# Kernel tuning notes

Hardware: AMD Instinct MI355X
Metric: run time of the kernel (lower is better)

Reference implementation:

```python
import jax, jax.numpy as jnp
import numpy as np

N, K, T, M, P = 16, 256, 1000, 384, 2
BN_EPS = 1e-3  # keras BatchNormalization default


def setup_inputs() -> dict:
    key = jax.random.key(0)
    ks = jax.random.split(key, 16)
    inp = {
        "V": jax.random.normal(ks[0], (N, K, M), dtype=jnp.float32),
        "duration_outputs": jax.random.normal(ks[1], (N, K), dtype=jnp.float32) * 0.5,
        # ConvBatchNorm params (Conv1D(8, kernel=3, same) + BN, inference mode)
        "conv_w": jax.random.normal(ks[2], (3, M, 8), dtype=jnp.float32) * 0.05,
        "conv_b": jnp.zeros((8,), dtype=jnp.float32),
        "bn_gamma": jnp.ones((8,), dtype=jnp.float32),
        "bn_beta": jnp.zeros((8,), dtype=jnp.float32),
        "bn_mean": jnp.zeros((8,), dtype=jnp.float32),
        "bn_var": jnp.ones((8,), dtype=jnp.float32),
        # score MLP: 10 -> 16 -> 16 -> 1
        "w1": jax.random.normal(ks[3], (10, 16), dtype=jnp.float32) * 0.3,
        "b1": jnp.zeros((16,), dtype=jnp.float32),
        "w2": jax.random.normal(ks[4], (16, 16), dtype=jnp.float32) * 0.25,
        "b2": jnp.zeros((16,), dtype=jnp.float32),
        "w3": jax.random.normal(ks[5], (16, 1), dtype=jnp.float32) * 0.25,
        "b3": jnp.zeros((1,), dtype=jnp.float32),
        # auxiliary MLP: 10 -> P -> P
        "aw1": jax.random.normal(ks[6], (10, P), dtype=jnp.float32) * 0.3,
        "ab1": jnp.zeros((P,), dtype=jnp.float32),
        "aw2": jax.random.normal(ks[7], (P, P), dtype=jnp.float32) * 0.5,
        "ab2": jnp.zeros((P,), dtype=jnp.float32),
        # projection P -> M (no bias)
        "proj_w": jax.random.normal(ks[8], (P, M), dtype=jnp.float32) * 0.05,
        "max_mel_length": T,
    }
    return inp


def _forward(V, duration_outputs, conv_w, conv_b, bn_gamma, bn_beta, bn_mean,
             bn_var, w1, b1, w2, b2, w3, b3, aw1, ab1, aw2, ab2, proj_w,
             max_mel_length):
    silu = jax.nn.silu
    # durations and start/end boundaries
    durations = jax.nn.relu(jnp.exp(duration_outputs) - 1.0)      # [N,K]
    S = jnp.cumsum(durations, axis=1) - durations                 # exclusive cumsum [N,K]
    E = S + durations                                             # [N,K]
    tgrid = jnp.arange(1, max_mel_length + 1, dtype=V.dtype)      # [T]
    S_mat = tgrid[None, :, None] - S[:, None, :]                  # [N,T,K]
    E_mat = E[:, None, :] - tgrid[None, :, None]                  # [N,T,K]
    # ConvBatchNorm on V (inference: BN uses moving stats, dropout is no-op)
    conv = jax.lax.conv_general_dilated(
        V, conv_w, window_strides=(1,), padding='SAME',
        dimension_numbers=('NWC', 'WIO', 'NWC')) + conv_b         # [N,K,8]
    conv = (conv - bn_mean) * jax.lax.rsqrt(bn_var + BN_EPS) * bn_gamma + bn_beta
    conv_V = silu(conv)                                           # [N,K,8]
    n, t, k = S_mat.shape
    conv_b4 = jnp.broadcast_to(conv_V[:, None, :, :], (n, t, k, conv_V.shape[-1]))
    W_input = jnp.concatenate(
        [S_mat[..., None], E_mat[..., None], conv_b4], axis=-1)   # [N,T,K,10]
    # score MLP + softmax over K
    h = silu(W_input @ w1 + b1)
    h = silu(h @ w2 + b2)
    score = (h @ w3 + b3)[..., 0]                                 # [N,T,K]
    W = jax.nn.softmax(score, axis=-1)
    # auxiliary MLP and weighted reduction
    C = silu(silu(W_input @ aw1 + ab1) @ aw2 + ab2)               # [N,T,K,P]
    proj_C = jnp.einsum('ntk,ntkp->ntp', W, C) @ proj_w           # [N,T,M]
    O = jnp.einsum('ntk,nkm->ntm', W, V) + proj_C                 # [N,T,M]
    return O


def reference(V, duration_outputs, conv_w, conv_b, bn_gamma, bn_beta, bn_mean,
              bn_var, w1, b1, w2, b2, w3, b3, aw1, ab1, aw2, ab2, proj_w,
              max_mel_length):
    return _forward(V, duration_outputs, conv_w, conv_b, bn_gamma, bn_beta,
                    bn_mean, bn_var, w1, b1, w2, b2, w3, b3, aw1, ab1, aw2,
                    ab2, proj_w, max_mel_length)
```

## Files before the change

kernel.cpp:

```cpp
#include <hip/hip_runtime.h>

#define NN 16
#define KK 256
#define TT 1000
#define MM 384
#define TCH 8
#define TOB 28
#define TP 1008
#define TPAD 1024

typedef short bf16x8 __attribute__((ext_vector_type(8)));
typedef float f32x4 __attribute__((ext_vector_type(4)));

__device__ __forceinline__ float fast_rcp(float x) { return __builtin_amdgcn_rcpf(x); }
__device__ __forceinline__ float silu_f(float x) {
    float e = __expf(-x);
    return x * fast_rcp(1.0f + e);
}
__device__ __forceinline__ unsigned short f2bf_rne(float f) {
    unsigned u = __float_as_uint(f);
    unsigned r = u + 0x7fff + ((u >> 16) & 1);
    return (unsigned short)(r >> 16);
}
__device__ __forceinline__ float bf2f(unsigned short h) {
    return __uint_as_float((unsigned)h << 16);
}

__global__ __launch_bounds__(256) void k_init(
    const float* __restrict__ dur_out, float* __restrict__ wsS,
    float* __restrict__ wsD, const float* __restrict__ V,
    unsigned short* __restrict__ Vth, unsigned short* __restrict__ Vtl,
    const float* __restrict__ conv_w, const float* __restrict__ conv_b,
    const float* __restrict__ bn_g, const float* __restrict__ bn_b,
    const float* __restrict__ bn_m, const float* __restrict__ bn_v,
    const float* __restrict__ w1, const float* __restrict__ b1,
    const float* __restrict__ aw1, const float* __restrict__ ab1,
    float* __restrict__ wsQ1, float* __restrict__ wsQA, int nvt) {
    __shared__ float shmem[8 * 3 * MM];
    int tid = threadIdx.x;
    int bid = blockIdx.x;

    if (bid < 16) {
        float* lds = shmem;
        int n = bid, k = tid;
        float d = __expf(dur_out[n * KK + k]) - 1.0f;
        d = fmaxf(d, 0.0f);
        lds[k] = d;
        __syncthreads();
        float run = d;
        for (int off = 1; off < KK; off <<= 1) {
            float v = (k >= off) ? lds[k - off] : 0.0f;
            __syncthreads();
            run += v;
            lds[k] = run;
            __syncthreads();
        }
        wsS[n * KK + k] = run - d;
        wsD[n * KK + k] = d;
    } else if (bid < 16 + nvt) {
        float (*tile)[65] = (float(*)[65])shmem;
        int id = bid - 16;
        int m0 = (id % 6) * 64;
        int k0 = ((id / 6) & 3) * 64;
        int n = id / 24;
        const float* Vn = V + (size_t)n * KK * MM;
        int mo = tid & 63, ks = tid >> 6;
        for (int kk = ks; kk < 64; kk += 4)
            tile[kk][mo] = Vn[(size_t)(k0 + kk) * MM + m0 + mo];
        __syncthreads();
        int ko = tid & 63, ms = tid >> 6;
        for (int mm = ms; mm < 64; mm += 4) {
            float v = tile[ko][mm];
            unsigned short hi = f2bf_rne(v);
            unsigned short lo = f2bf_rne(v - bf2f(hi));
            size_t o = ((size_t)n * MM + m0 + mm) * KK + k0 + ko;
            Vth[o] = hi;
            Vtl[o] = lo;
        }
    } else {
        float* wt = shmem;
        int id = bid - 16 - nvt;
        int kcb = id & 63;
        int n = id >> 6;
        for (int i = tid; i < 3 * MM * 8; i += 256) {
            int tap = i / (MM * 8);
            int r = i - tap * (MM * 8);
            int m = r >> 3, c = r & 7;
            wt[(c * 3 + tap) * MM + m] = conv_w[i];
        }
        __syncthreads();

        int wv = tid >> 6, lane = tid & 63;
        int k = kcb * 4 + wv;
        const float* Vn = V + (size_t)n * KK * MM;

        float p[8];
#pragma unroll
        for (int c = 0; c < 8; ++c) p[c] = 0.f;

#pragma unroll
        for (int tap = 0; tap < 3; ++tap) {
            int kk = k + tap - 1;
            if (kk < 0 || kk >= KK) continue;
            const float* vrow = Vn + (size_t)kk * MM;
#pragma unroll
            for (int j = 0; j < 6; ++j) {
                int m = lane + 64 * j;
                float v = vrow[m];
#pragma unroll
                for (int c = 0; c < 8; ++c)
                    p[c] = fmaf(v, wt[(c * 3 + tap) * MM + m], p[c]);
            }
        }
#pragma unroll
        for (int c = 0; c < 8; ++c) {
#pragma unroll
            for (int off = 32; off >= 1; off >>= 1) p[c] += __shfl_xor(p[c], off);
        }
        float cv[8];
#pragma unroll
        for (int c = 0; c < 8; ++c) {
            float xx = p[c] + conv_b[c];
            float bn = (xx - bn_m[c]) * (bn_g[c] * rsqrtf(bn_v[c] + 1e-3f)) + bn_b[c];
            cv[c] = silu_f(bn);
        }
        float d = fmaxf(__expf(dur_out[n * KK + k]) - 1.0f, 0.0f);
        if (lane < 16) {
            int j = lane;
            float q = fmaf(d, w1[16 + j], b1[j]);
#pragma unroll
            for (int c = 0; c < 8; ++c) q = fmaf(cv[c], w1[(2 + c) * 16 + j], q);
            wsQ1[((size_t)(n * KK + k)) * 16 + j] = q;
        } else if (lane < 18) {
            int pp = lane - 16;
            float q = fmaf(d, aw1[2 + pp], ab1[pp]);
#pragma unroll
            for (int c = 0; c < 8; ++c) q = fmaf(cv[c], aw1[(2 + c) * 2 + pp], q);
            wsQA[(size_t)(n * KK + k) * 2 + pp] = q;
        }
    }
}

__global__ __launch_bounds__(256) void k_score(
    const float* __restrict__ w1, const float* __restrict__ w2g,
    const float* __restrict__ b2g, const float* __restrict__ w3g,
    const float* __restrict__ b3g, const float* __restrict__ aw1,
    const float* __restrict__ aw2g, const float* __restrict__ ab2g,
    const float* __restrict__ wsS, const float* __restrict__ wsQ1,
    const float* __restrict__ wsQA, float* __restrict__ wcg,
    float* __restrict__ ETf, unsigned short* __restrict__ ETh,
    unsigned short* __restrict__ ETl, int use_bf16) {
    __shared__ __align__(16) float sc[TCH * KK];
    __shared__ __align__(16) float rl[16];

    int tid = threadIdx.x;
    int tb = blockIdx.x * TCH;
    int n = blockIdx.y;
    int nK = n * KK;

    if (tid < 16) rl[tid] = w1[tid] - w1[16 + tid];

    float b3v = b3g[0];
    float b2r[16];
    {
        const float4* bp = (const float4*)b2g;
#pragma unroll
        for (int g = 0; g < 4; ++g) {
            float4 b = bp[g];
            b2r[4 * g + 0] = b.x; b2r[4 * g + 1] = b.y;
            b2r[4 * g + 2] = b.z; b2r[4 * g + 3] = b.w;
        }
    }
    int k = tid;
    float S_k = wsS[nK + k];
    float q1[16];
    {
        const float4* q1p = (const float4*)&wsQ1[(size_t)(nK + k) * 16];
#pragma unroll
        for (int g = 0; g < 4; ++g) {
            float4 qv = q1p[g];
            q1[4 * g + 0] = qv.x; q1[4 * g + 1] = qv.y;
            q1[4 * g + 2] = qv.z; q1[4 * g + 3] = qv.w;
        }
    }
    __syncthreads();

    for (int tq = 0; tq < TCH / 4; ++tq) {
        float s0 = (float)(tb + 4 * tq + 1) - S_k;
        float aA[16], aB[16], aC[16], aD[16];
#pragma unroll
        for (int j = 0; j < 16; ++j) {
            aA[j] = b2r[j]; aB[j] = b2r[j]; aC[j] = b2r[j]; aD[j] = b2r[j];
        }
#pragma unroll
        for (int j1 = 0; j1 < 16; ++j1) {
            float r = rl[j1];
            float q = q1[j1];
            float hA = silu_f(fmaf(s0, r, q));
            float hB = silu_f(fmaf(s0 + 1.0f, r, q));
            float hC = silu_f(fmaf(s0 + 2.0f, r, q));
            float hD = silu_f(fmaf(s0 + 3.0f, r, q));
            const float4* wr = (const float4*)&w2g[j1 * 16];
#pragma unroll
            for (int g = 0; g < 4; ++g) {
                float4 w = wr[g];
                aA[4 * g + 0] = fmaf(hA, w.x, aA[4 * g + 0]);
                aA[4 * g + 1] = fmaf(hA, w.y, aA[4 * g + 1]);
                aA[4 * g + 2] = fmaf(hA, w.z, aA[4 * g + 2]);
                aA[4 * g + 3] = fmaf(hA, w.w, aA[4 * g + 3]);
                aB[4 * g + 0] = fmaf(hB, w.x, aB[4 * g + 0]);
                aB[4 * g + 1] = fmaf(hB, w.y, aB[4 * g + 1]);
                aB[4 * g + 2] = fmaf(hB, w.z, aB[4 * g + 2]);
                aB[4 * g + 3] = fmaf(hB, w.w, aB[4 * g + 3]);
                aC[4 * g + 0] = fmaf(hC, w.x, aC[4 * g + 0]);
                aC[4 * g + 1] = fmaf(hC, w.y, aC[4 * g + 1]);
                aC[4 * g + 2] = fmaf(hC, w.z, aC[4 * g + 2]);
                aC[4 * g + 3] = fmaf(hC, w.w, aC[4 * g + 3]);
                aD[4 * g + 0] = fmaf(hD, w.x, aD[4 * g + 0]);
                aD[4 * g + 1] = fmaf(hD, w.y, aD[4 * g + 1]);
                aD[4 * g + 2] = fmaf(hD, w.z, aD[4 * g + 2]);
                aD[4 * g + 3] = fmaf(hD, w.w, aD[4 * g + 3]);
            }
        }
        float scA = b3v, scB = b3v, scC = b3v, scD = b3v;
#pragma unroll
        for (int g = 0; g < 4; ++g) {
            float4 wq = *(const float4*)&w3g[4 * g];
            scA = fmaf(silu_f(aA[4 * g + 0]), wq.x, scA);
            scA = fmaf(silu_f(aA[4 * g + 1]), wq.y, scA);
            scA = fmaf(silu_f(aA[4 * g + 2]), wq.z, scA);
            scA = fmaf(silu_f(aA[4 * g + 3]), wq.w, scA);
            scB = fmaf(silu_f(aB[4 * g + 0]), wq.x, scB);
            scB = fmaf(silu_f(aB[4 * g + 1]), wq.y, scB);
            scB = fmaf(silu_f(aB[4 * g + 2]), wq.z, scB);
            scB = fmaf(silu_f(aB[4 * g + 3]), wq.w, scB);
            scC = fmaf(silu_f(aC[4 * g + 0]), wq.x, scC);
            scC = fmaf(silu_f(aC[4 * g + 1]), wq.y, scC);
            scC = fmaf(silu_f(aC[4 * g + 2]), wq.z, scC);
            scC = fmaf(silu_f(aC[4 * g + 3]), wq.w, scC);
            scD = fmaf(silu_f(aD[4 * g + 0]), wq.x, scD);
            scD = fmaf(silu_f(aD[4 * g + 1]), wq.y, scD);
            scD = fmaf(silu_f(aD[4 * g + 2]), wq.z, scD);
            scD = fmaf(silu_f(aD[4 * g + 3]), wq.w, scD);
        }
        sc[(4 * tq + 0) * KK + k] = scA;
        sc[(4 * tq + 1) * KK + k] = scB;
        sc[(4 * tq + 2) * KK + k] = scC;
        sc[(4 * tq + 3) * KK + k] = scD;
    }
    __syncthreads();

    {
        float rA0 = aw1[0] - aw1[2];
        float rA1 = aw1[1] - aw1[3];
        float aw200 = aw2g[0], aw201 = aw2g[1], aw210 = aw2g[2], aw211 = aw2g[3];
        float ab20 = ab2g[0], ab21 = ab2g[1];
        int wv = tid >> 6, lane = tid & 63;
        float S4[4]; float2 QA4[4];
#pragma unroll
        for (int j = 0; j < 4; ++j) {
            int kk2 = lane + 64 * j;
            S4[j] = wsS[nK + kk2];
            QA4[j] = *(const float2*)&wsQA[(size_t)(nK + kk2) * 2];
        }
#pragma unroll
        for (int i = 0; i < 2; ++i) {
            int t = wv * 2 + i;
            int tt = tb + t;
            float v0 = sc[t * KK + lane];
            float v1 = sc[t * KK + lane + 64];
            float v2 = sc[t * KK + lane + 128];
            float v3 = sc[t * KK + lane + 192];
            float mx = fmaxf(fmaxf(v0, v1), fmaxf(v2, v3));
#pragma unroll
            for (int off = 32; off >= 1; off >>= 1) mx = fmaxf(mx, __shfl_xor(mx, off));
            float e0 = __expf(v0 - mx), e1 = __expf(v1 - mx);
            float e2 = __expf(v2 - mx), e3 = __expf(v3 - mx);
            float ssum = e0 + e1 + e2 + e3;
            float wc0 = 0.f, wc1 = 0.f;
            float tc = (float)(tt + 1);
            float ear[4] = {e0, e1, e2, e3};
#pragma unroll
            for (int j = 0; j < 4; ++j) {
                float s = tc - S4[j];
                float a0 = silu_f(fmaf(s, rA0, QA4[j].x));
                float a1 = silu_f(fmaf(s, rA1, QA4[j].y));
                float c0 = silu_f(fmaf(a1, aw210, fmaf(a0, aw200, ab20)));
                float c1 = silu_f(fmaf(a1, aw211, fmaf(a0, aw201, ab21)));
                wc0 = fmaf(ear[j], c0, wc0);
                wc1 = fmaf(ear[j], c1, wc1);
            }
#pragma unroll
            for (int off = 32; off >= 1; off >>= 1) {
                ssum += __shfl_xor(ssum, off);
                wc0 += __shfl_xor(wc0, off);
                wc1 += __shfl_xor(wc1, off);
            }
            float inv = fast_rcp(ssum);
            sc[t * KK + lane]       = e0 * inv;
            sc[t * KK + lane + 64]  = e1 * inv;
            sc[t * KK + lane + 128] = e2 * inv;
            sc[t * KK + lane + 192] = e3 * inv;
            if (lane == 0) {
                wcg[(size_t)(n * TT + tt) * 2]     = wc0 * inv;
                wcg[(size_t)(n * TT + tt) * 2 + 1] = wc1 * inv;
            }
        }
    }
    __syncthreads();

    if (use_bf16) {
#pragma unroll
        for (int t2 = 0; t2 < TCH; ++t2) {
            float e = sc[t2 * KK + k];
            unsigned short hi = f2bf_rne(e);
            unsigned short lo = f2bf_rne(e - bf2f(hi));
            size_t o = ((size_t)n * TPAD + tb + t2) * KK + k;
            ETh[o] = hi;
            ETl[o] = lo;
        }
    } else {
        for (int idx = tid; idx < TCH * KK; idx += 256) {
            int k2 = idx >> 3, t2 = idx & 7;
            ETf[((size_t)(nK + k2)) * TP + tb + t2] = sc[t2 * KK + k2];
        }
    }
}

__global__ __launch_bounds__(384) void k_gemm(
    const unsigned short* __restrict__ ETh, const unsigned short* __restrict__ ETl,
    const unsigned short* __restrict__ Vth, const unsigned short* __restrict__ Vtl,
    const float* __restrict__ wcg, const float* __restrict__ projw,
    float* __restrict__ out) {
    int tid = threadIdx.x;
    int w = tid >> 6, lane = tid & 63;
    int tb = blockIdx.x * 32;
    int n = blockIdx.y;
    int r16 = lane & 15, kh = lane >> 4;
    int mb = w * 64;

    const unsigned short* eh0 = ETh + ((size_t)n * TPAD + tb + r16) * KK + kh * 8;
    const unsigned short* el0 = ETl + ((size_t)n * TPAD + tb + r16) * KK + kh * 8;
    const unsigned short* vh0 = Vth + ((size_t)n * MM + mb + r16) * KK + kh * 8;
    const unsigned short* vl0 = Vtl + ((size_t)n * MM + mb + r16) * KK + kh * 8;

    f32x4 acc[2][4];
#pragma unroll
    for (int tt = 0; tt < 2; ++tt)
#pragma unroll
        for (int mm = 0; mm < 4; ++mm) acc[tt][mm] = (f32x4){0.f, 0.f, 0.f, 0.f};

#pragma unroll
    for (int kb = 0; kb < 8; ++kb) {
        int ko = kb * 32;
        bf16x8 ah0 = *(const bf16x8*)(eh0 + ko);
        bf16x8 ah1 = *(const bf16x8*)(eh0 + 16 * KK + ko);
        bf16x8 al0 = *(const bf16x8*)(el0 + ko);
        bf16x8 al1 = *(const bf16x8*)(el0 + 16 * KK + ko);
#pragma unroll
        for (int mm = 0; mm < 4; ++mm) {
            bf16x8 bh = *(const bf16x8*)(vh0 + (size_t)mm * 16 * KK + ko);
            bf16x8 bl = *(const bf16x8*)(vl0 + (size_t)mm * 16 * KK + ko);
            acc[0][mm] = __builtin_amdgcn_mfma_f32_16x16x32_bf16(ah0, bh, acc[0][mm], 0, 0, 0);
            acc[0][mm] = __builtin_amdgcn_mfma_f32_16x16x32_bf16(ah0, bl, acc[0][mm], 0, 0, 0);
            acc[0][mm] = __builtin_amdgcn_mfma_f32_16x16x32_bf16(al0, bh, acc[0][mm], 0, 0, 0);
            acc[1][mm] = __builtin_amdgcn_mfma_f32_16x16x32_bf16(ah1, bh, acc[1][mm], 0, 0, 0);
            acc[1][mm] = __builtin_amdgcn_mfma_f32_16x16x32_bf16(ah1, bl, acc[1][mm], 0, 0, 0);
            acc[1][mm] = __builtin_amdgcn_mfma_f32_16x16x32_bf16(al1, bh, acc[1][mm], 0, 0, 0);
        }
    }

#pragma unroll
    for (int tt = 0; tt < 2; ++tt) {
#pragma unroll
        for (int r = 0; r < 4; ++r) {
            int t = tb + tt * 16 + kh * 4 + r;
            if (t < TT) {
                float c0 = wcg[(size_t)(n * TT + t) * 2];
                float c1 = wcg[(size_t)(n * TT + t) * 2 + 1];
#pragma unroll
                for (int mm = 0; mm < 4; ++mm) {
                    int m = mb + mm * 16 + r16;
                    float pw0 = projw[m], pw1 = projw[MM + m];
                    out[((size_t)n * TT + t) * MM + m] =
                        acc[tt][mm][r] + c0 * pw0 + c1 * pw1;
                }
            }
        }
    }
}

__global__ __launch_bounds__(384) void k_out(
    const float* __restrict__ V, const float* __restrict__ projw,
    const float* __restrict__ wcg, const float* __restrict__ ET,
    float* __restrict__ out) {
    int tid = threadIdx.x;
    int tb = blockIdx.x * TOB;
    int n = blockIdx.y;
    int nK = n * KK;
    const float* Vn = V + (size_t)n * KK * MM;
    const float* Eb = ET + (size_t)nK * TP + tb;
    int m = tid;

    float acc[TOB];
#pragma unroll
    for (int t = 0; t < TOB; ++t) acc[t] = 0.f;

    for (int kx = 0; kx < KK; ++kx) {
        const float4* ep = (const float4*)(Eb + (size_t)kx * TP);
        float vv = Vn[(size_t)kx * MM + m];
#pragma unroll
        for (int q = 0; q < TOB / 4; ++q) {
            float4 e = ep[q];
            acc[4 * q + 0] = fmaf(e.x, vv, acc[4 * q + 0]);
            acc[4 * q + 1] = fmaf(e.y, vv, acc[4 * q + 1]);
            acc[4 * q + 2] = fmaf(e.z, vv, acc[4 * q + 2]);
            acc[4 * q + 3] = fmaf(e.w, vv, acc[4 * q + 3]);
        }
    }

    float pw0 = projw[m], pw1 = projw[MM + m];
#pragma unroll
    for (int t = 0; t < TOB; ++t) {
        int tt = tb + t;
        if (tt < TT) {
            float c0 = wcg[(size_t)(n * TT + tt) * 2];
            float c1 = wcg[(size_t)(n * TT + tt) * 2 + 1];
            out[((size_t)n * TT + tt) * MM + m] = acc[t] + c0 * pw0 + c1 * pw1;
        }
    }
}

extern "C" void kernel_launch(void* const* d_in, const int* in_sizes, int n_in,
                              void* d_out, int out_size, void* d_ws, size_t ws_size,
                              hipStream_t stream) {
    const float* V   = (const float*)d_in[0];
    const float* dur = (const float*)d_in[1];
    const float* cw  = (const float*)d_in[2];
    const float* cb  = (const float*)d_in[3];
    const float* bng = (const float*)d_in[4];
    const float* bnb = (const float*)d_in[5];
    const float* bnm = (const float*)d_in[6];
    const float* bnv = (const float*)d_in[7];
    const float* w1  = (const float*)d_in[8];
    const float* b1  = (const float*)d_in[9];
    const float* w2  = (const float*)d_in[10];
    const float* b2  = (const float*)d_in[11];
    const float* w3  = (const float*)d_in[12];
    const float* b3  = (const float*)d_in[13];
    const float* aw1 = (const float*)d_in[14];
    const float* ab1 = (const float*)d_in[15];
    const float* aw2 = (const float*)d_in[16];
    const float* ab2 = (const float*)d_in[17];
    const float* pw  = (const float*)d_in[18];
    float* out = (float*)d_out;
    float* ws = (float*)d_ws;

    float* wsS  = ws;
    float* wsD  = ws + 4096;
    float* wsQ1 = ws + 8192;
    float* wsQA = ws + 73728;
    float* wcg  = ws + 81920;
    char*  base = (char*)(ws + 114688);

    size_t sz_ETh = (size_t)NN * TPAD * KK * 2;
    size_t sz_Vt  = (size_t)NN * MM * KK * 2;
    size_t need   = 114688 * 4 + 2 * sz_ETh + 2 * sz_Vt;
    bool mfma_path = (ws_size >= need);

    if (mfma_path) {
        unsigned short* ETh = (unsigned short*)base;
        unsigned short* ETl = (unsigned short*)(base + sz_ETh);
        unsigned short* Vth = (unsigned short*)(base + 2 * sz_ETh);
        unsigned short* Vtl = (unsigned short*)(base + 2 * sz_ETh + sz_Vt);
        int nvt = 6 * 4 * NN;
        hipLaunchKernelGGL(k_init, dim3(16 + nvt + 64 * NN), dim3(256), 0, stream,
                           dur, wsS, wsD, V, Vth, Vtl, cw, cb, bng, bnb, bnm, bnv,
                           w1, b1, aw1, ab1, wsQ1, wsQA, nvt);
        hipLaunchKernelGGL(k_score, dim3(TT / TCH, NN), dim3(256), 0,
                           stream, w1, w2, b2, w3, b3, aw1, aw2, ab2, wsS, wsQ1,
                           wsQA, wcg, (float*)nullptr, ETh, ETl, 1);
        hipLaunchKernelGGL(k_gemm, dim3(TPAD / 32, NN), dim3(384), 0, stream,
                           ETh, ETl, Vth, Vtl, wcg, pw, out);
    } else {
        float* ETf = (float*)base;
        hipLaunchKernelGGL(k_init, dim3(16 + 64 * NN), dim3(256), 0, stream,
                           dur, wsS, wsD, V, (unsigned short*)nullptr,
                           (unsigned short*)nullptr, cw, cb, bng, bnb, bnm, bnv,
                           w1, b1, aw1, ab1, wsQ1, wsQA, 0);
        hipLaunchKernelGGL(k_score, dim3(TT / TCH, NN), dim3(256), 0,
                           stream, w1, w2, b2, w3, b3, aw1, aw2, ab2, wsS, wsQ1,
                           wsQA, wcg, ETf, (unsigned short*)nullptr,
                           (unsigned short*)nullptr, 0);
        hipLaunchKernelGGL(k_out, dim3((TT + TOB - 1) / TOB, NN), dim3(384), 0,
                           stream, V, pw, wcg, ETf, out);
    }
}
```

Baseline: 130.8 us.

## Reuse exp across time steps in score MLP, stage conv rows in LDS, remap gemm grid

The score kernel now computes one exp per hidden unit per group of four time steps and gets the other three by multiplying by a precomputed exp(-r), instead of calling exp four times. The conv branch of the init kernel loads the six neighbouring V rows into shared memory once and reads all three taps from there, rather than each wave reading global memory. The gemm kernel moves to a 1D grid whose block-to-(n,t) mapping places each batch on the same XCD so V tiles are reused in its L2. The unused duration buffer write is also removed; the chained exp products may lose a little accuracy or overflow when the argument is large.

```diff
diff --git a/kernel.cpp b/kernel.cpp
--- a/kernel.cpp
+++ b/kernel.cpp
@@ -28,7 +28,7 @@
 
 __global__ __launch_bounds__(256) void k_init(
     const float* __restrict__ dur_out, float* __restrict__ wsS,
-    float* __restrict__ wsD, const float* __restrict__ V,
+    const float* __restrict__ V,
     unsigned short* __restrict__ Vth, unsigned short* __restrict__ Vtl,
     const float* __restrict__ conv_w, const float* __restrict__ conv_b,
     const float* __restrict__ bn_g, const float* __restrict__ bn_b,
@@ -36,7 +36,7 @@
     const float* __restrict__ w1, const float* __restrict__ b1,
     const float* __restrict__ aw1, const float* __restrict__ ab1,
     float* __restrict__ wsQ1, float* __restrict__ wsQA, int nvt) {
-    __shared__ float shmem[8 * 3 * MM];
+    __shared__ float shmem[8 * 3 * MM + 6 * MM];
     int tid = threadIdx.x;
     int bid = blockIdx.x;
 
@@ -56,7 +56,6 @@
             __syncthreads();
         }
         wsS[n * KK + k] = run - d;
-        wsD[n * KK + k] = d;
     } else if (bid < 16 + nvt) {
         float (*tile)[65] = (float(*)[65])shmem;
         int id = bid - 16;
@@ -79,20 +78,27 @@
         }
     } else {
         float* wt = shmem;
+        float* vrows = shmem + 8 * 3 * MM;
         int id = bid - 16 - nvt;
         int kcb = id & 63;
         int n = id >> 6;
+        int k0 = kcb * 4;
+        const float* Vn = V + (size_t)n * KK * MM;
         for (int i = tid; i < 3 * MM * 8; i += 256) {
             int tap = i / (MM * 8);
             int r = i - tap * (MM * 8);
             int m = r >> 3, c = r & 7;
             wt[(c * 3 + tap) * MM + m] = conv_w[i];
         }
+        for (int i = tid; i < 6 * MM; i += 256) {
+            int row = i / MM, m = i - row * MM;
+            int kk = k0 - 1 + row;
+            vrows[i] = (kk >= 0 && kk < KK) ? Vn[(size_t)kk * MM + m] : 0.f;
+        }
         __syncthreads();
 
         int wv = tid >> 6, lane = tid & 63;
-        int k = kcb * 4 + wv;
-        const float* Vn = V + (size_t)n * KK * MM;
+        int k = k0 + wv;
 
         float p[8];
 #pragma unroll
@@ -100,9 +106,7 @@
 
 #pragma unroll
         for (int tap = 0; tap < 3; ++tap) {
-            int kk = k + tap - 1;
-            if (kk < 0 || kk >= KK) continue;
-            const float* vrow = Vn + (size_t)kk * MM;
+            const float* vrow = vrows + (wv + tap) * MM;
 #pragma unroll
             for (int j = 0; j < 6; ++j) {
                 int m = lane + 64 * j;
@@ -185,6 +189,10 @@
     }
     __syncthreads();
 
+    float er[16];
+#pragma unroll
+    for (int j = 0; j < 16; ++j) er[j] = __expf(-rl[j]);
+
     for (int tq = 0; tq < TCH / 4; ++tq) {
         float s0 = (float)(tb + 4 * tq + 1) - S_k;
         float aA[16], aB[16], aC[16], aD[16];
@@ -196,10 +204,19 @@
         for (int j1 = 0; j1 < 16; ++j1) {
             float r = rl[j1];
             float q = q1[j1];
-            float hA = silu_f(fmaf(s0, r, q));
-            float hB = silu_f(fmaf(s0 + 1.0f, r, q));
-            float hC = silu_f(fmaf(s0 + 2.0f, r, q));
-            float hD = silu_f(fmaf(s0 + 3.0f, r, q));
+            float uA = fmaf(s0, r, q);
+            float uB = uA + r;
+            float uC = uB + r;
+            float uD = uC + r;
+            float ej = er[j1];
+            float eA = __expf(-uA);
+            float eB = eA * ej;
+            float eC = eB * ej;
+            float eD = eC * ej;
+            float hA = uA * fast_rcp(1.0f + eA);
+            float hB = uB * fast_rcp(1.0f + eB);
+            float hC = uC * fast_rcp(1.0f + eC);
+            float hD = uD * fast_rcp(1.0f + eD);
             const float4* wr = (const float4*)&w2g[j1 * 16];
 #pragma unroll
             for (int g = 0; g < 4; ++g) {
@@ -334,8 +351,11 @@
     float* __restrict__ out) {
     int tid = threadIdx.x;
     int w = tid >> 6, lane = tid & 63;
-    int tb = blockIdx.x * 32;
-    int n = blockIdx.y;
+    int id = blockIdx.x;
+    int xcd = id & 7;
+    int tmp = id >> 3;
+    int n = xcd + ((tmp >> 5) << 3);
+    int tb = (tmp & 31) * 32;
     int r16 = lane & 15, kh = lane >> 4;
     int mb = w * 64;
 
@@ -457,7 +477,6 @@
     float* ws = (float*)d_ws;
 
     float* wsS  = ws;
-    float* wsD  = ws + 4096;
     float* wsQ1 = ws + 8192;
     float* wsQA = ws + 73728;
     float* wcg  = ws + 81920;
@@ -475,17 +494,17 @@
         unsigned short* Vtl = (unsigned short*)(base + 2 * sz_ETh + sz_Vt);
         int nvt = 6 * 4 * NN;
         hipLaunchKernelGGL(k_init, dim3(16 + nvt + 64 * NN), dim3(256), 0, stream,
-                           dur, wsS, wsD, V, Vth, Vtl, cw, cb, bng, bnb, bnm, bnv,
+                           dur, wsS, V, Vth, Vtl, cw, cb, bng, bnb, bnm, bnv,
                            w1, b1, aw1, ab1, wsQ1, wsQA, nvt);
         hipLaunchKernelGGL(k_score, dim3(TT / TCH, NN), dim3(256), 0,
                            stream, w1, w2, b2, w3, b3, aw1, aw2, ab2, wsS, wsQ1,
                            wsQA, wcg, (float*)nullptr, ETh, ETl, 1);
-        hipLaunchKernelGGL(k_gemm, dim3(TPAD / 32, NN), dim3(384), 0, stream,
+        hipLaunchKernelGGL(k_gemm, dim3((TPAD / 32) * NN), dim3(384), 0, stream,
                            ETh, ETl, Vth, Vtl, wcg, pw, out);
     } else {
         float* ETf = (float*)base;
         hipLaunchKernelGGL(k_init, dim3(16 + 64 * NN), dim3(256), 0, stream,
-                           dur, wsS, wsD, V, (unsigned short*)nullptr,
+                           dur, wsS, V, (unsigned short*)nullptr,
                            (unsigned short*)nullptr, cw, cb, bng, bnb, bnm, bnv,
                            w1, b1, aw1, ab1, wsQ1, wsQA, 0);
         hipLaunchKernelGGL(k_score, dim3(TT / TCH, NN), dim3(256), 0,
```

Result: slower. 134.6 us (+2.9%).
